# Optimization experiments

Hardware: AMD Instinct MI355X
Metric: run time of the kernel (lower is better)

The kernel has to match this reference:

```python
import jax, jax.numpy as jnp
import numpy as np

N = 4096; TD = 768; ID = 512; H = 256; NH = 4; HD = H // NH; NC = 3; E = 131072


def _gcn(x, w, b, src, dst, n):
    # GCNConv: add self loops, sym-normalize, aggregate at dst
    loop = jnp.arange(n)
    s = jnp.concatenate([src, loop])
    d = jnp.concatenate([dst, loop])
    deg = jax.ops.segment_sum(jnp.ones(s.shape[0], x.dtype), d, num_segments=n)
    dinv = jnp.where(deg > 0, jax.lax.rsqrt(deg), 0.0)
    norm = dinv[s] * dinv[d]                      # [E+N]
    h = x @ w                                     # [N,H] transform
    out = jax.ops.segment_sum(norm[:, None] * h[s], d, num_segments=n)
    return out + b


def setup_inputs() -> dict:
    key = jax.random.key(0)
    ks = jax.random.split(key, 20)
    p = lambda k, shp, sc: jax.random.normal(k, shp, jnp.float32) * sc
    inp = {
        "text_features": jax.random.normal(ks[0], (N, TD), jnp.float32),
        "image_features": jax.random.normal(ks[1], (N, ID), jnp.float32),
        "edge_index": jax.random.randint(ks[2], (2, E), 0, N, jnp.int32),
        "text_w": p(ks[3], (TD, H), 0.02), "text_b": jnp.zeros((H,), jnp.float32),
        "image_w": p(ks[4], (ID, H), 0.02), "image_b": jnp.zeros((H,), jnp.float32),
        "wq": p(ks[5], (H, H), 0.02), "bq": jnp.zeros((H,), jnp.float32),
        "wk": p(ks[6], (H, H), 0.02), "bk": jnp.zeros((H,), jnp.float32),
        "wv": p(ks[7], (H, H), 0.02), "bv": jnp.zeros((H,), jnp.float32),
        "wo": p(ks[8], (H, H), 0.02), "bo": jnp.zeros((H,), jnp.float32),
        "gcn1_w": p(ks[9], (H, H), 0.02), "gcn1_b": jnp.zeros((H,), jnp.float32),
        "gcn2_w": p(ks[10], (H, H), 0.02), "gcn2_b": jnp.zeros((H,), jnp.float32),
        "cls_w": p(ks[11], (H, NC), 0.02), "cls_b": jnp.zeros((NC,), jnp.float32),
    }
    return inp


def reference(text_features, image_features, edge_index,
              text_w, text_b, image_w, image_b,
              wq, bq, wk, bk, wv, bv, wo, bo,
              gcn1_w, gcn1_b, gcn2_w, gcn2_b, cls_w, cls_b):
    # fused linear+relu projections, then elementwise fuse of sum
    combined = (jax.nn.relu(text_features @ text_w + text_b)
                + jax.nn.relu(image_features @ image_w + image_b))  # [N,H]
    # MHA over all nodes (seq_len=N, batch=1)
    q = (combined @ wq + bq).reshape(N, NH, HD)
    k = (combined @ wk + bk).reshape(N, NH, HD)
    v = (combined @ wv + bv).reshape(N, NH, HD)
    scores = jnp.einsum('nhd,mhd->hnm', q, k) / jnp.sqrt(jnp.float32(HD))
    attn = jax.nn.softmax(scores, axis=-1)
    o = jnp.einsum('hnm,mhd->nhd', attn, v).reshape(N, H)
    attn_out = o @ wo + bo
    # two GCN layers
    src, dst = edge_index[0], edge_index[1]
    g1 = jax.nn.relu(_gcn(attn_out, gcn1_w, gcn1_b, src, dst, N))
    g2 = _gcn(g1, gcn2_w, gcn2_b, src, dst, N)
    return g2 @ cls_w + cls_b
```

## Files before the change

### kernel.cpp

```cpp
#include <hip/hip_runtime.h>
#include <hip/hip_bf16.h>

typedef unsigned short ushort;
typedef __attribute__((ext_vector_type(8))) short short8;
typedef __attribute__((ext_vector_type(4))) float f32x4;

constexpr int N_  = 4096;
constexpr int TD_ = 768;
constexpr int ID_ = 512;
constexpr int H_  = 256;
constexpr int HD_ = 64;
constexpr int E_  = 131072;
constexpr int SPLITS = 16;
constexpr float QSCALE = 0.125f * 1.44269504088896f;

#define MFMA16(a, b, c) __builtin_amdgcn_mfma_f32_16x16x32_bf16(a, b, c, 0, 0, 0)

__device__ inline ushort f2bf(float x) {
    union { float f; unsigned u; } v; v.f = x;
    unsigned r = v.u + 0x7fff + ((v.u >> 16) & 1);
    return (ushort)(r >> 16);
}
__device__ inline float lo2f(unsigned u) { union { unsigned x; float f; } v; v.x = u << 16; return v.f; }
__device__ inline float hi2f(unsigned u) { union { unsigned x; float f; } v; v.x = u & 0xffff0000u; return v.f; }

__device__ inline float exp2r(float x) {
    float r;
    asm("v_exp_f32 %0, %1" : "=v"(r) : "v"(x));
    return r;
}
__device__ inline unsigned pkbf(float lo, float hi) {
    union { float f; unsigned u; } a, b; a.f = lo; b.f = hi;
    return __builtin_amdgcn_perm(b.u + 0x8000u, a.u + 0x8000u, 0x07060302u);
}

__device__ inline void gl_lds16(const void* g, void* l) {
    __builtin_amdgcn_global_load_lds((const __attribute__((address_space(1))) unsigned int*)g,
                                     (__attribute__((address_space(3))) unsigned int*)l, 16, 0, 0);
}

__device__ inline void stage64(const ushort* g, long long strideEl, ushort* lds, int w, int l) {
    int r8 = l >> 3;
    int cc = (l & 7) ^ r8;
    #pragma unroll
    for (int p = 0; p < 2; p++) {
        int row = w * 16 + p * 8 + r8;
        gl_lds16(g + (long long)row * strideEl + cc * 8, lds + (w * 16 + p * 8) * 64);
    }
}
__device__ inline void stageB16(const ushort* g, long long strideEl, ushort* lds, int w, int l) {
    if (w < 2) {
        int r8 = l >> 3;
        int row = w * 8 + r8;
        int cc = (l & 7) ^ (row & 7);
        gl_lds16(g + (long long)row * strideEl + cc * 8, lds + w * 512);
    }
}
__device__ inline int swz(int row, int kOff) {
    return row * 64 + ((((kOff >> 3) ^ (row & 7))) << 3);
}


__global__ __launch_bounds__(256) void k_init(int* __restrict__ indeg, int* __restrict__ pos) {
    int i = blockIdx.x * 256 + threadIdx.x;
    indeg[i] = 0;
    pos[i] = 0;
}


__global__ __launch_bounds__(256) void k_prep(const float* __restrict__ text, const float* __restrict__ img,
                                              const float* __restrict__ tw, const float* __restrict__ iw,
                                              const float* __restrict__ wq, const float* __restrict__ wk,
                                              const float* __restrict__ wv, const float* __restrict__ wo,
                                              const float* __restrict__ g1w, const float* __restrict__ g2w,
                                              const int* __restrict__ edst, int* __restrict__ indeg,
                                              ushort* __restrict__ textbf, ushort* __restrict__ imgbf,
                                              ushort* __restrict__ wobf,
                                              ushort* __restrict__ twT, ushort* __restrict__ iwT,
                                              ushort* __restrict__ wqT, ushort* __restrict__ wkT,
                                              ushort* __restrict__ wvT, ushort* __restrict__ g1wT,
                                              ushort* __restrict__ g2wT) {
    __shared__ float Ts[64][65];
    const int b = blockIdx.x;
    const int t = threadIdx.x;
    if (b >= 2752) {
        int e = (b - 2752) * 256 + t;
        atomicAdd(&indeg[edst[e]], 1);
        return;
    }
    if (b < 2592) {
        size_t base = ((size_t)b * 256 + t) * 8;
        const size_t TXE = (size_t)N_ * TD_, IME = (size_t)N_ * ID_;
        const float* src; ushort* dst;
        if (base < TXE) { src = text + base; dst = textbf + base; }
        else if (base < TXE + IME) { src = img + (base - TXE); dst = imgbf + (base - TXE); }
        else { src = wo + (base - TXE - IME); dst = wobf + (base - TXE - IME); }
        float4 x = *(const float4*)src;
        float4 y = *(const float4*)(src + 4);
        ushort o[8] = { f2bf(x.x), f2bf(x.y), f2bf(x.z), f2bf(x.w),
                        f2bf(y.x), f2bf(y.y), f2bf(y.z), f2bf(y.w) };
        *(short8*)dst = *(const short8*)o;
        return;
    }
    int wb = b - 2592;
    const float* src; ushort* dst; int R, tile;
    if (wb < 48)       { src = tw;  dst = twT;  R = 768; tile = wb; }
    else if (wb < 80)  { src = iw;  dst = iwT;  R = 512; tile = wb - 48; }
    else if (wb < 96)  { src = wq;  dst = wqT;  R = 256; tile = wb - 80; }
    else if (wb < 112) { src = wk;  dst = wkT;  R = 256; tile = wb - 96; }
    else if (wb < 128) { src = wv;  dst = wvT;  R = 256; tile = wb - 112; }
    else if (wb < 144) { src = g1w; dst = g1wT; R = 256; tile = wb - 128; }
    else               { src = g2w; dst = g2wT; R = 256; tile = wb - 144; }
    const int r0 = (tile >> 2) * 64, c0 = (tile & 3) * 64;
    #pragma unroll
    for (int u = 0; u < 16; u++) {
        int lin = t + u * 256;
        int r = lin >> 6, c = lin & 63;
        Ts[r][c] = src[(size_t)(r0 + r) * 256 + c0 + c];
    }
    __syncthreads();
    #pragma unroll
    for (int u = 0; u < 16; u++) {
        int lin = t + u * 256;
        int c = lin >> 6, r = lin & 63;
        dst[(size_t)(c0 + c) * R + r0 + r] = f2bf(Ts[r][c]);
    }
}


__global__ __launch_bounds__(256, 4) void k_combined16(const ushort* __restrict__ text, const ushort* __restrict__ img,
                                                       const ushort* __restrict__ twT, const ushort* __restrict__ iwT,
                                                       const float* __restrict__ tb, const float* __restrict__ ib,
                                                       const int* __restrict__ indeg, int* __restrict__ offs,
                                                       float* __restrict__ dinv, ushort* __restrict__ out) {
    __shared__ ushort As[2][4096];
    __shared__ ushort Bs[2][1024];
    __shared__ ushort Cs[64 * 24];
    __shared__ int sums[256];
    const int b = blockIdx.x;
    const int t = threadIdx.x;
    if (b == 1024) {
        int v[16]; int ssum = 0; int base = t * 16;
        #pragma unroll
        for (int k2 = 0; k2 < 16; k2++) { v[k2] = indeg[base + k2]; ssum += v[k2]; }
        sums[t] = ssum;
        __syncthreads();
        for (int off = 1; off < 256; off <<= 1) {
            int x = (t >= off) ? sums[t - off] : 0;
            __syncthreads();
            sums[t] += x;
            __syncthreads();
        }
        int excl = sums[t] - ssum;
        #pragma unroll
        for (int k2 = 0; k2 < 16; k2++) {
            offs[base + k2] = excl;
            excl += v[k2];
            dinv[base + k2] = 1.f / sqrtf((float)(v[k2] + 1));
        }
        return;
    }
    const int bm = (b >> 4) * 64, bn = (b & 15) * 16;
    const int w = t >> 6, l = t & 63, q = l >> 4, i = l & 15;
    f32x4 acc1 = {0, 0, 0, 0}, acc2 = {0, 0, 0, 0};
    auto stC = [&](int c, int buf) {
        if (c < 12) {
            stage64(text + (size_t)bm * TD_ + c * 64, TD_, As[buf], w, l);
            stageB16(twT + (size_t)bn * TD_ + c * 64, TD_, Bs[buf], w, l);
        } else {
            stage64(img + (size_t)bm * ID_ + (c - 12) * 64, ID_, As[buf], w, l);
            stageB16(iwT + (size_t)bn * ID_ + (c - 12) * 64, ID_, Bs[buf], w, l);
        }
    };
    stC(0, 0);
    for (int c = 0; c < 20; c++) {
        __syncthreads();
        if (c + 1 < 20) stC(c + 1, (c + 1) & 1);
        const ushort* Ab = As[c & 1];
        const ushort* Bb = Bs[c & 1];
        #pragma unroll
        for (int kb = 0; kb < 2; kb++) {
            short8 af = *(const short8*)&Ab[swz(w * 16 + i, kb * 32 + q * 8)];
            short8 bfr = *(const short8*)&Bb[swz(i, kb * 32 + q * 8)];
            if (c < 12) acc1 = MFMA16(af, bfr, acc1);
            else        acc2 = MFMA16(af, bfr, acc2);
        }
    }
    __syncthreads();
    float b1 = tb[bn + i], b2 = ib[bn + i];
    #pragma unroll
    for (int r = 0; r < 4; r++) {
        float v = fmaxf(acc1[r] + b1, 0.f) + fmaxf(acc2[r] + b2, 0.f);
        Cs[(w * 16 + q * 4 + r) * 24 + i] = f2bf(v);
    }
    __syncthreads();
    if (t < 128) {
        int row = t >> 1, h8 = (t & 1) * 8;
        *(short8*)(out + (size_t)(bm + row) * H_ + bn + h8) = *(const short8*)&Cs[row * 24 + h8];
    }
}


__global__ __launch_bounds__(256) void k_qkv_scatfold(const ushort* __restrict__ A,
                                                      const ushort* __restrict__ WqT, const ushort* __restrict__ WkT,
                                                      const ushort* __restrict__ WvT,
                                                      const float* __restrict__ bq, const float* __restrict__ bk,
                                                      const float* __restrict__ bv,
                                                      ushort* __restrict__ Qg, ushort* __restrict__ Kg,
                                                      ushort* __restrict__ Vtg,
                                                      const int* __restrict__ esrc, const int* __restrict__ edst,
                                                      const int* __restrict__ offs, const float* __restrict__ dinv,
                                                      int* __restrict__ pos, int* __restrict__ ssrc,
                                                      float* __restrict__ swv,
                                                      const ushort* __restrict__ g1wT, const ushort* __restrict__ wobf,
                                                      const float* __restrict__ bo,
                                                      ushort* __restrict__ WpT, float* __restrict__ bp) {
    __shared__ ushort As[2][4096];
    __shared__ ushort Bs[2][4096];
    __shared__ ushort Cs[64 * 72];
    const int b = blockIdx.x;
    const int t = threadIdx.x;
    const int w = t >> 6, l = t & 63, q = l >> 4, i = l & 15;

    if (b >= 768) {
        if (b < 1280) {
            int e = (b - 768) * 256 + t;
            int s = esrc[e], d = edst[e];
            int p = atomicAdd(&pos[d], 1);
            int idx = offs[d] + p;
            ssrc[idx] = s;
            swv[idx] = dinv[s] * dinv[d];
            return;
        }
        if (b == 1296) {
            float acc = 0.f;
            const ushort* row = g1wT + (size_t)t * 256;
            for (int m8 = 0; m8 < 256; m8 += 8) {
                #pragma unroll
                for (int j = 0; j < 8; j++) acc += bo[m8 + j] * lo2f(((unsigned)row[m8 + j]) << 16);
            }
            bp[t] = acc;
            return;
        }
        const int f = b - 1280;
        const int bm = (f >> 2) * 64, bn = (f & 3) * 64;
        f32x4 acc[4];
        #pragma unroll
        for (int nt = 0; nt < 4; nt++) acc[nt] = (f32x4){0, 0, 0, 0};
        stage64(g1wT + (size_t)bm * H_, H_, As[0], w, l);
        stage64(wobf + (size_t)bn * H_, H_, Bs[0], w, l);
        for (int c = 0; c < 4; c++) {
            __syncthreads();
            if (c < 3) {
                stage64(g1wT + (size_t)bm * H_ + (c + 1) * 64, H_, As[(c + 1) & 1], w, l);
                stage64(wobf + (size_t)bn * H_ + (c + 1) * 64, H_, Bs[(c + 1) & 1], w, l);
            }
            const ushort* Ab = As[c & 1];
            const ushort* Bb = Bs[c & 1];
            #pragma unroll
            for (int kb = 0; kb < 2; kb++) {
                short8 af = *(const short8*)&Ab[swz(w * 16 + i, kb * 32 + q * 8)];
                #pragma unroll
                for (int nt = 0; nt < 4; nt++) {
                    short8 bfr = *(const short8*)&Bb[swz(nt * 16 + i, kb * 32 + q * 8)];
                    acc[nt] = MFMA16(af, bfr, acc[nt]);
                }
            }
        }
        __syncthreads();
        #pragma unroll
        for (int nt = 0; nt < 4; nt++)
            #pragma unroll
            for (int r = 0; r < 4; r++)
                Cs[(w * 16 + q * 4 + r) * 72 + nt * 16 + i] = f2bf(acc[nt][r]);
        __syncthreads();
        int rr = t >> 2, c16 = (t & 3) * 16;
        short8 v0 = *(const short8*)&Cs[rr * 72 + c16];
        short8 v1 = *(const short8*)&Cs[rr * 72 + c16 + 8];
        ushort* dstp = WpT + (size_t)(bm + rr) * H_ + bn + c16;
        *(short8*)dstp = v0;
        *(short8*)(dstp + 8) = v1;
        return;
    }

    const int z = b >> 8, rem = b & 255;
    const int bm = (rem >> 2) * 64, head = rem & 3;
    const ushort* WT = (z == 0) ? WqT : (z == 1) ? WkT : WvT;
    const float* bias = (z == 0) ? bq : (z == 1) ? bk : bv;
    f32x4 acc[4];
    #pragma unroll
    for (int nt = 0; nt < 4; nt++) acc[nt] = (f32x4){0, 0, 0, 0};

    stage64(A + (size_t)bm * H_, H_, As[0], w, l);
    stage64(WT + (size_t)(head * 64) * H_, H_, Bs[0], w, l);
    for (int c = 0; c < 4; c++) {
        __syncthreads();
        if (c < 3) {
            stage64(A + (size_t)bm * H_ + (c + 1) * 64, H_, As[(c + 1) & 1], w, l);
            stage64(WT + (size_t)(head * 64) * H_ + (c + 1) * 64, H_, Bs[(c + 1) & 1], w, l);
        }
        const ushort* Ab = As[c & 1];
        const ushort* Bb = Bs[c & 1];
        #pragma unroll
        for (int kb = 0; kb < 2; kb++) {
            short8 af = *(const short8*)&Ab[swz(w * 16 + i, kb * 32 + q * 8)];
            #pragma unroll
            for (int nt = 0; nt < 4; nt++) {
                short8 bfr = *(const short8*)&Bb[swz(nt * 16 + i, kb * 32 + q * 8)];
                acc[nt] = MFMA16(af, bfr, acc[nt]);
            }
        }
    }
    __syncthreads();
    #pragma unroll
    for (int nt = 0; nt < 4; nt++) {
        float bv_ = bias[head * 64 + nt * 16 + i];
        #pragma unroll
        for (int r = 0; r < 4; r++) {
            float v = acc[nt][r] + bv_;
            if (z == 0) v *= QSCALE;
            if (z < 2) Cs[(w * 16 + q * 4 + r) * 72 + nt * 16 + i] = f2bf(v);
            else       Cs[(nt * 16 + i) * 72 + w * 16 + q * 4 + r] = f2bf(v);
        }
    }
    __syncthreads();
    int rr = t >> 2, c16 = (t & 3) * 16;
    short8 v0 = *(const short8*)&Cs[rr * 72 + c16];
    short8 v1 = *(const short8*)&Cs[rr * 72 + c16 + 8];
    ushort* dst;
    if (z < 2) dst = ((z == 0) ? Qg : Kg) + (size_t)head * N_ * HD_ + (size_t)(bm + rr) * HD_ + c16;
    else       dst = Vtg + (size_t)head * HD_ * N_ + (size_t)rr * N_ + bm + c16;
    *(short8*)dst = v0;
    *(short8*)(dst + 8) = v1;
}


__global__ __launch_bounds__(256) void k_attn_mfma(const ushort* __restrict__ Qg, const ushort* __restrict__ Kg,
                                                   const ushort* __restrict__ Vtg, ushort* __restrict__ Op,
                                                   float* __restrict__ lp) {
    __shared__ ushort Ks[4096];
    __shared__ ushort Vs[4096];
    __shared__ ushort Ps[4][16 * 72];
    const int head = blockIdx.y, r0 = blockIdx.x * 128, z = blockIdx.z;
    const int t = threadIdx.x, w = t >> 6, l = t & 63, q = l >> 4, i = l & 15;
    const int rw = (i ^ (i >> 1)) & 7;
    ushort* Pw = &Ps[w][0];

    short8 qf[2][2];
    #pragma unroll
    for (int qt = 0; qt < 2; qt++)
        #pragma unroll
        for (int kb = 0; kb < 2; kb++)
            qf[qt][kb] = *(const short8*)(Qg + ((size_t)head * N_ + r0 + qt * 64 + w * 16 + i) * HD_ + kb * 32 + q * 8);

    f32x4 Oacc[2][4];
    float lacc[2] = {0.f, 0.f};
    #pragma unroll
    for (int qt = 0; qt < 2; qt++)
        #pragma unroll
        for (int dt = 0; dt < 4; dt++) Oacc[qt][dt] = (f32x4){0, 0, 0, 0};

    const int NT = 64 / SPLITS;
    const int cb0 = z * NT;
    for (int it = 0; it < NT; it++) {
        const int cb = cb0 + it;
        __syncthreads();
        stage64(Kg + ((size_t)head * N_ + (size_t)cb * 64) * HD_, HD_, Ks, w, l);
        stage64(Vtg + (size_t)head * HD_ * N_ + cb * 64, N_, Vs, w, l);
        __syncthreads();

        f32x4 St[2][4];
        #pragma unroll
        for (int qt = 0; qt < 2; qt++)
            #pragma unroll
            for (int kt = 0; kt < 4; kt++) St[qt][kt] = (f32x4){0, 0, 0, 0};
        #pragma unroll
        for (int kb = 0; kb < 2; kb++) {
            #pragma unroll
            for (int kt = 0; kt < 4; kt++) {
                short8 kf = *(const short8*)&Ks[swz(kt * 16 + i, kb * 32 + q * 8)];
                St[0][kt] = MFMA16(kf, qf[0][kb], St[0][kt]);
                St[1][kt] = MFMA16(kf, qf[1][kb], St[1][kt]);
            }
        }
        #pragma unroll
        for (int qt = 0; qt < 2; qt++) {
            #pragma unroll
            for (int kt = 0; kt < 4; kt++) {
                float p0 = exp2r(St[qt][kt][0]), p1 = exp2r(St[qt][kt][1]);
                float p2 = exp2r(St[qt][kt][2]), p3 = exp2r(St[qt][kt][3]);
                lacc[qt] += (p0 + p1) + (p2 + p3);
                int off = i * 72 + (((2 * kt + (q >> 1)) ^ rw) << 3) + ((q & 1) << 2);
                uint2 v; v.x = pkbf(p0, p1); v.y = pkbf(p2, p3);
                *(uint2*)&Pw[off] = v;
            }
            #pragma unroll
            for (int kb = 0; kb < 2; kb++) {
                short8 pf = *(const short8*)&Pw[i * 72 + (((4 * kb + q) ^ rw) << 3)];
                #pragma unroll
                for (int dt = 0; dt < 4; dt++) {
                    short8 vf = *(const short8*)&Vs[swz(dt * 16 + i, kb * 32 + q * 8)];
                    Oacc[qt][dt] = MFMA16(vf, pf, Oacc[qt][dt]);
                }
            }
        }
    }

    #pragma unroll
    for (int qt = 0; qt < 2; qt++) {
        lacc[qt] += __shfl_xor(lacc[qt], 16);
        lacc[qt] += __shfl_xor(lacc[qt], 32);
    }

    const size_t sh = ((size_t)z * 4 + head) * N_;
    #pragma unroll
    for (int qt = 0; qt < 2; qt++) {
        const int row = r0 + qt * 64 + w * 16 + i;
        #pragma unroll
        for (int dt = 0; dt < 4; dt++) {
            uint2 v;
            v.x = pkbf(Oacc[qt][dt][0], Oacc[qt][dt][1]);
            v.y = pkbf(Oacc[qt][dt][2], Oacc[qt][dt][3]);
            *(uint2*)&Op[(sh + row) * HD_ + dt * 16 + q * 4] = v;
        }
        if (l < 16) lp[sh + r0 + qt * 64 + w * 16 + l] = lacc[qt];
    }
}

__global__ __launch_bounds__(256) void k_attn_merge(const ushort* __restrict__ Op, const float* __restrict__ lp,
                                                    ushort* __restrict__ obuf) {
    const int t = threadIdx.x;
    const int idx = blockIdx.x * 16 + (t >> 4);
    const int h = idx >> 12, n = idx & 4095;
    const int d4 = (t & 15) * 4;
    float lsum = 0.f;
    float acc[4] = {0.f, 0.f, 0.f, 0.f};
    #pragma unroll
    for (int s = 0; s < SPLITS; s++) {
        size_t sh = ((size_t)s * 4 + h) * N_ + n;
        lsum += lp[sh];
        uint2 o4 = *(const uint2*)&Op[sh * HD_ + d4];
        acc[0] += lo2f(o4.x); acc[1] += hi2f(o4.x);
        acc[2] += lo2f(o4.y); acc[3] += hi2f(o4.y);
    }
    float inv = 1.f / lsum;
    uint2 res;
    res.x = pkbf(acc[0] * inv, acc[1] * inv);
    res.y = pkbf(acc[2] * inv, acc[3] * inv);
    *(uint2*)&obuf[(size_t)n * H_ + h * HD_ + d4] = res;
}


template <bool BIAS>
__global__ __launch_bounds__(256, 4) void k_gemm16(const ushort* __restrict__ A, const ushort* __restrict__ BT,
                                                   const float* __restrict__ bias, ushort* __restrict__ outb) {
    __shared__ ushort As[2][4096];
    __shared__ ushort Bs[2][1024];
    __shared__ ushort Cs[64 * 24];
    const int bm = blockIdx.x * 64, bn = blockIdx.y * 16;
    const int t = threadIdx.x, w = t >> 6, l = t & 63, q = l >> 4, i = l & 15;
    f32x4 acc = {0, 0, 0, 0};
    stage64(A + (size_t)bm * H_, H_, As[0], w, l);
    stageB16(BT + (size_t)bn * H_, H_, Bs[0], w, l);
    for (int c = 0; c < 4; c++) {
        __syncthreads();
        if (c < 3) {
            stage64(A + (size_t)bm * H_ + (c + 1) * 64, H_, As[(c + 1) & 1], w, l);
            stageB16(BT + (size_t)bn * H_ + (c + 1) * 64, H_, Bs[(c + 1) & 1], w, l);
        }
        const ushort* Ab = As[c & 1];
        const ushort* Bb = Bs[c & 1];
        #pragma unroll
        for (int kb = 0; kb < 2; kb++) {
            short8 af = *(const short8*)&Ab[swz(w * 16 + i, kb * 32 + q * 8)];
            short8 bfr = *(const short8*)&Bb[swz(i, kb * 32 + q * 8)];
            acc = MFMA16(af, bfr, acc);
        }
    }
    __syncthreads();
    float bb = BIAS ? bias[bn + i] : 0.f;
    #pragma unroll
    for (int r = 0; r < 4; r++)
        Cs[(w * 16 + q * 4 + r) * 24 + i] = f2bf(acc[r] + bb);
    __syncthreads();
    if (t < 128) {
        int row = t >> 1, h8 = (t & 1) * 8;
        *(short8*)(outb + (size_t)(bm + row) * H_ + bn + h8) = *(const short8*)&Cs[row * 24 + h8];
    }
}


__global__ __launch_bounds__(256) void k_agg1(const ushort* __restrict__ h, const int* __restrict__ ssrc,
                                              const float* __restrict__ sw, const int* __restrict__ offs,
                                              const int* __restrict__ indeg, const float* __restrict__ dinv,
                                              const float* __restrict__ bias, ushort* __restrict__ outb) {
    const int t = threadIdx.x;
    const int j = __builtin_amdgcn_readfirstlane(blockIdx.x * 4 + (t >> 6));
    const int d0 = (t & 63) * 4;
    float dj = dinv[j];
    uint2 hv = *(const uint2*)&h[(size_t)j * H_ + d0];
    float s2 = dj * dj;
    float a0 = s2 * lo2f(hv.x), a1 = s2 * hi2f(hv.x), a2 = s2 * lo2f(hv.y), a3 = s2 * hi2f(hv.y);
    int start = offs[j], cnt = indeg[j];
    for (int e = 0; e < cnt; e++) {
        int s = ssrc[start + e];
        float wg = sw[start + e];
        uint2 v = *(const uint2*)&h[(size_t)s * H_ + d0];
        a0 += wg * lo2f(v.x); a1 += wg * hi2f(v.x);
        a2 += wg * lo2f(v.y); a3 += wg * hi2f(v.y);
    }
    a0 = fmaxf(a0 + bias[d0], 0.f);
    a1 = fmaxf(a1 + bias[d0 + 1], 0.f);
    a2 = fmaxf(a2 + bias[d0 + 2], 0.f);
    a3 = fmaxf(a3 + bias[d0 + 3], 0.f);
    uint2 o;
    o.x = pkbf(a0, a1);
    o.y = pkbf(a2, a3);
    *(uint2*)&outb[(size_t)j * H_ + d0] = o;
}


__global__ __launch_bounds__(256) void k_aggcls(const ushort* __restrict__ h, const int* __restrict__ ssrc,
                                                const float* __restrict__ sw, const int* __restrict__ offs,
                                                const int* __restrict__ indeg, const float* __restrict__ dinv,
                                                const float* __restrict__ bias, const float* __restrict__ cw,
                                                const float* __restrict__ cb, float* __restrict__ out) {
    const int t = threadIdx.x;
    const int j = __builtin_amdgcn_readfirstlane(blockIdx.x * 4 + (t >> 6));
    const int lane = t & 63;
    const int d0 = lane * 4;
    float dj = dinv[j];
    uint2 hv = *(const uint2*)&h[(size_t)j * H_ + d0];
    float s2 = dj * dj;
    float a0 = s2 * lo2f(hv.x), a1 = s2 * hi2f(hv.x), a2 = s2 * lo2f(hv.y), a3 = s2 * hi2f(hv.y);
    int start = offs[j], cnt = indeg[j];
    for (int e = 0; e < cnt; e++) {
        int s = ssrc[start + e];
        float wg = sw[start + e];
        uint2 v = *(const uint2*)&h[(size_t)s * H_ + d0];
        a0 += wg * lo2f(v.x); a1 += wg * hi2f(v.x);
        a2 += wg * lo2f(v.y); a3 += wg * hi2f(v.y);
    }
    a0 += bias[d0]; a1 += bias[d0 + 1]; a2 += bias[d0 + 2]; a3 += bias[d0 + 3];
    float p0 = a0 * cw[d0 * 3 + 0] + a1 * cw[(d0 + 1) * 3 + 0]
             + a2 * cw[(d0 + 2) * 3 + 0] + a3 * cw[(d0 + 3) * 3 + 0];
    float p1 = a0 * cw[d0 * 3 + 1] + a1 * cw[(d0 + 1) * 3 + 1]
             + a2 * cw[(d0 + 2) * 3 + 1] + a3 * cw[(d0 + 3) * 3 + 1];
    float p2 = a0 * cw[d0 * 3 + 2] + a1 * cw[(d0 + 1) * 3 + 2]
             + a2 * cw[(d0 + 2) * 3 + 2] + a3 * cw[(d0 + 3) * 3 + 2];
    #pragma unroll
    for (int off = 32; off > 0; off >>= 1) {
        p0 += __shfl_xor(p0, off);
        p1 += __shfl_xor(p1, off);
        p2 += __shfl_xor(p2, off);
    }
    if (lane == 0) {
        out[j * 3 + 0] = p0 + cb[0];
        out[j * 3 + 1] = p1 + cb[1];
        out[j * 3 + 2] = p2 + cb[2];
    }
}


extern "C" void kernel_launch(void* const* d_in, const int* in_sizes, int n_in,
                              void* d_out, int out_size, void* d_ws, size_t ws_size,
                              hipStream_t stream) {
    const float* text = (const float*)d_in[0];
    const float* img  = (const float*)d_in[1];
    const int*   eidx = (const int*)d_in[2];
    const float* tw  = (const float*)d_in[3];
    const float* tb  = (const float*)d_in[4];
    const float* iw  = (const float*)d_in[5];
    const float* ib  = (const float*)d_in[6];
    const float* wq  = (const float*)d_in[7];
    const float* bq  = (const float*)d_in[8];
    const float* wk  = (const float*)d_in[9];
    const float* bk  = (const float*)d_in[10];
    const float* wv  = (const float*)d_in[11];
    const float* bv  = (const float*)d_in[12];
    const float* wo  = (const float*)d_in[13];
    const float* bo  = (const float*)d_in[14];
    const float* g1w = (const float*)d_in[15];
    const float* g1b = (const float*)d_in[16];
    const float* g2w = (const float*)d_in[17];
    const float* g2b = (const float*)d_in[18];
    const float* cw  = (const float*)d_in[19];
    const float* cbv = (const float*)d_in[20];

    char* W = (char*)d_ws;
    size_t cur = 0;
    auto alloc = [&](size_t sz) { char* p = W + cur; cur += (sz + 255) & ~(size_t)255; return p; };

    float* dinv  = (float*)alloc(N_ * 4);
    float* swv   = (float*)alloc(E_ * 4);
    int* indeg   = (int*)alloc(N_ * 4);
    int* offs    = (int*)alloc(N_ * 4);
    int* pos     = (int*)alloc(N_ * 4);
    int* ssrc    = (int*)alloc(E_ * 4);
    ushort* Qg   = (ushort*)alloc((size_t)N_ * H_ * 2);
    ushort* Kg   = (ushort*)alloc((size_t)N_ * H_ * 2);
    ushort* Vtg  = (ushort*)alloc((size_t)N_ * H_ * 2);
    ushort* obuf = (ushort*)alloc((size_t)N_ * H_ * 2);
    ushort* WpT  = (ushort*)alloc((size_t)H_ * H_ * 2);
    float* bp    = (float*)alloc(H_ * 4);
    ushort* g1wT = (ushort*)alloc((size_t)H_ * H_ * 2);
    ushort* g2wT = (ushort*)alloc((size_t)H_ * H_ * 2);
    ushort* wobf = (ushort*)alloc((size_t)H_ * H_ * 2);
    float* lp    = (float*)alloc((size_t)SPLITS * 4 * N_ * 4);
    char* S = W + cur;

    ushort* textbf = (ushort*)S;
    ushort* imgbf  = textbf + (size_t)N_ * TD_;
    ushort* twT    = imgbf + (size_t)N_ * ID_;
    ushort* iwT    = twT + (size_t)TD_ * H_;
    ushort* wqT    = iwT + (size_t)ID_ * H_;
    ushort* wkT    = wqT + (size_t)H_ * H_;
    ushort* wvT    = wkT + (size_t)H_ * H_;
    ushort* combbf = wvT + (size_t)H_ * H_;
    ushort* Op = (ushort*)S;
    ushort* hbuf  = (ushort*)S;
    ushort* g1b16 = (ushort*)(S + (size_t)2 * 1024 * 1024);
    ushort* hbuf2 = (ushort*)(S + (size_t)4 * 1024 * 1024);

    const int* esrc = eidx;
    const int* edst = eidx + E_;

    k_init<<<dim3(N_ / 256), dim3(256), 0, stream>>>(indeg, pos);
    k_prep<<<dim3(3264), dim3(256), 0, stream>>>(text, img, tw, iw, wq, wk, wv, wo, g1w, g2w,
                                                 edst, indeg,
                                                 textbf, imgbf, wobf, twT, iwT, wqT, wkT, wvT, g1wT, g2wT);
    k_combined16<<<dim3(1025), dim3(256), 0, stream>>>(textbf, imgbf, twT, iwT, tb, ib,
                                                       indeg, offs, dinv, combbf);
    k_qkv_scatfold<<<dim3(1297), dim3(256), 0, stream>>>(combbf, wqT, wkT, wvT, bq, bk, bv, Qg, Kg, Vtg,
                                                         esrc, edst, offs, dinv, pos, ssrc, swv,
                                                         g1wT, wobf, bo, WpT, bp);
    k_attn_mfma<<<dim3(32, 4, SPLITS), dim3(256), 0, stream>>>(Qg, Kg, Vtg, Op, lp);
    k_attn_merge<<<dim3(1024), dim3(256), 0, stream>>>(Op, lp, obuf);

    k_gemm16<true><<<dim3(64, 16), dim3(256), 0, stream>>>(obuf, WpT, bp, hbuf);
    k_agg1<<<dim3(N_ / 4), dim3(256), 0, stream>>>(hbuf, ssrc, swv, offs, indeg, dinv, g1b, g1b16);
    k_gemm16<false><<<dim3(64, 16), dim3(256), 0, stream>>>(g1b16, g2wT, nullptr, hbuf2);
    k_aggcls<<<dim3(N_ / 4), dim3(256), 0, stream>>>(hbuf2, ssrc, swv, offs, indeg, dinv, g2b, cw, cbv,
                                                     (float*)d_out);
}
```

Measured before the change: 228.6 us.

## Widen combined-projection GEMM tiles and double-buffer K staging in attention

The text/image projection GEMM now gives each block a 64x64 output tile instead of 64x16. That cuts the grid from 1024 to 256 blocks, so each A tile is staged once and reused across four MFMA column tiles rather than being reloaded by sixteen blocks. The attention kernel now double-buffers the K tile and stages V for the current block after the loop-top barrier. A new barrier sits before the P·V product, so the V load can overlap the QK^T MFMAs. The trade-offs are more accumulator registers and LDS in the GEMM, fewer blocks to fill the GPU, and an extra barrier per attention iteration.

```diff
diff --git a/kernel.cpp b/kernel.cpp
--- a/kernel.cpp
+++ b/kernel.cpp
@@ -128,18 +128,18 @@
 }
 
 
-__global__ __launch_bounds__(256, 4) void k_combined16(const ushort* __restrict__ text, const ushort* __restrict__ img,
-                                                       const ushort* __restrict__ twT, const ushort* __restrict__ iwT,
-                                                       const float* __restrict__ tb, const float* __restrict__ ib,
-                                                       const int* __restrict__ indeg, int* __restrict__ offs,
-                                                       float* __restrict__ dinv, ushort* __restrict__ out) {
+__global__ __launch_bounds__(256) void k_combined16(const ushort* __restrict__ text, const ushort* __restrict__ img,
+                                                    const ushort* __restrict__ twT, const ushort* __restrict__ iwT,
+                                                    const float* __restrict__ tb, const float* __restrict__ ib,
+                                                    const int* __restrict__ indeg, int* __restrict__ offs,
+                                                    float* __restrict__ dinv, ushort* __restrict__ out) {
     __shared__ ushort As[2][4096];
-    __shared__ ushort Bs[2][1024];
-    __shared__ ushort Cs[64 * 24];
+    __shared__ ushort Bs[2][4096];
+    __shared__ ushort Cs[64 * 72];
     __shared__ int sums[256];
     const int b = blockIdx.x;
     const int t = threadIdx.x;
-    if (b == 1024) {
+    if (b == 256) {
         int v[16]; int ssum = 0; int base = t * 16;
         #pragma unroll
         for (int k2 = 0; k2 < 16; k2++) { v[k2] = indeg[base + k2]; ssum += v[k2]; }
@@ -160,16 +160,18 @@
         }
         return;
     }
-    const int bm = (b >> 4) * 64, bn = (b & 15) * 16;
+    const int bm = (b >> 2) * 64, bn = (b & 3) * 64;
     const int w = t >> 6, l = t & 63, q = l >> 4, i = l & 15;
-    f32x4 acc1 = {0, 0, 0, 0}, acc2 = {0, 0, 0, 0};
+    f32x4 acc1[4], acc2[4];
+    #pragma unroll
+    for (int nt = 0; nt < 4; nt++) { acc1[nt] = (f32x4){0, 0, 0, 0}; acc2[nt] = (f32x4){0, 0, 0, 0}; }
     auto stC = [&](int c, int buf) {
         if (c < 12) {
             stage64(text + (size_t)bm * TD_ + c * 64, TD_, As[buf], w, l);
-            stageB16(twT + (size_t)bn * TD_ + c * 64, TD_, Bs[buf], w, l);
+            stage64(twT + (size_t)bn * TD_ + c * 64, TD_, Bs[buf], w, l);
         } else {
             stage64(img + (size_t)bm * ID_ + (c - 12) * 64, ID_, As[buf], w, l);
-            stageB16(iwT + (size_t)bn * ID_ + (c - 12) * 64, ID_, Bs[buf], w, l);
+            stage64(iwT + (size_t)bn * ID_ + (c - 12) * 64, ID_, Bs[buf], w, l);
         }
     };
     stC(0, 0);
@@ -181,23 +183,31 @@
         #pragma unroll
         for (int kb = 0; kb < 2; kb++) {
             short8 af = *(const short8*)&Ab[swz(w * 16 + i, kb * 32 + q * 8)];
-            short8 bfr = *(const short8*)&Bb[swz(i, kb * 32 + q * 8)];
-            if (c < 12) acc1 = MFMA16(af, bfr, acc1);
-            else        acc2 = MFMA16(af, bfr, acc2);
+            #pragma unroll
+            for (int nt = 0; nt < 4; nt++) {
+                short8 bfr = *(const short8*)&Bb[swz(nt * 16 + i, kb * 32 + q * 8)];
+                if (c < 12) acc1[nt] = MFMA16(af, bfr, acc1[nt]);
+                else        acc2[nt] = MFMA16(af, bfr, acc2[nt]);
+            }
         }
     }
     __syncthreads();
-    float b1 = tb[bn + i], b2 = ib[bn + i];
-    #pragma unroll
-    for (int r = 0; r < 4; r++) {
-        float v = fmaxf(acc1[r] + b1, 0.f) + fmaxf(acc2[r] + b2, 0.f);
-        Cs[(w * 16 + q * 4 + r) * 24 + i] = f2bf(v);
+    #pragma unroll
+    for (int nt = 0; nt < 4; nt++) {
+        float b1 = tb[bn + nt * 16 + i], b2 = ib[bn + nt * 16 + i];
+        #pragma unroll
+        for (int r = 0; r < 4; r++) {
+            float v = fmaxf(acc1[nt][r] + b1, 0.f) + fmaxf(acc2[nt][r] + b2, 0.f);
+            Cs[(w * 16 + q * 4 + r) * 72 + nt * 16 + i] = f2bf(v);
+        }
     }
     __syncthreads();
-    if (t < 128) {
-        int row = t >> 1, h8 = (t & 1) * 8;
-        *(short8*)(out + (size_t)(bm + row) * H_ + bn + h8) = *(const short8*)&Cs[row * 24 + h8];
-    }
+    int rr = t >> 2, c16 = (t & 3) * 16;
+    short8 v0 = *(const short8*)&Cs[rr * 72 + c16];
+    short8 v1 = *(const short8*)&Cs[rr * 72 + c16 + 8];
+    ushort* dstp = out + (size_t)(bm + rr) * H_ + bn + c16;
+    *(short8*)dstp = v0;
+    *(short8*)(dstp + 8) = v1;
 }
 
 
@@ -338,7 +348,7 @@
 __global__ __launch_bounds__(256) void k_attn_mfma(const ushort* __restrict__ Qg, const ushort* __restrict__ Kg,
                                                    const ushort* __restrict__ Vtg, ushort* __restrict__ Op,
                                                    float* __restrict__ lp) {
-    __shared__ ushort Ks[4096];
+    __shared__ ushort Ks[2][4096];
     __shared__ ushort Vs[4096];
     __shared__ ushort Ps[4][16 * 72];
     const int head = blockIdx.y, r0 = blockIdx.x * 128, z = blockIdx.z;
@@ -362,12 +372,17 @@
 
     const int NT = 64 / SPLITS;
     const int cb0 = z * NT;
+    const ushort* Kbase = Kg + (size_t)head * N_ * HD_;
+    const ushort* Vbase = Vtg + (size_t)head * HD_ * N_;
+
+    stage64(Kbase + (size_t)cb0 * 64 * HD_, HD_, Ks[0], w, l);
     for (int it = 0; it < NT; it++) {
         const int cb = cb0 + it;
         __syncthreads();
-        stage64(Kg + ((size_t)head * N_ + (size_t)cb * 64) * HD_, HD_, Ks, w, l);
-        stage64(Vtg + (size_t)head * HD_ * N_ + cb * 64, N_, Vs, w, l);
-        __syncthreads();
+        stage64(Vbase + cb * 64, N_, Vs, w, l);
+        if (it + 1 < NT)
+            stage64(Kbase + (size_t)(cb + 1) * 64 * HD_, HD_, Ks[(it + 1) & 1], w, l);
+        const ushort* Kb = Ks[it & 1];
 
         f32x4 St[2][4];
         #pragma unroll
@@ -378,30 +393,46 @@
         for (int kb = 0; kb < 2; kb++) {
             #pragma unroll
             for (int kt = 0; kt < 4; kt++) {
-                short8 kf = *(const short8*)&Ks[swz(kt * 16 + i, kb * 32 + q * 8)];
+                short8 kf = *(const short8*)&Kb[swz(kt * 16 + i, kb * 32 + q * 8)];
                 St[0][kt] = MFMA16(kf, qf[0][kb], St[0][kt]);
                 St[1][kt] = MFMA16(kf, qf[1][kb], St[1][kt]);
             }
         }
         #pragma unroll
-        for (int qt = 0; qt < 2; qt++) {
-            #pragma unroll
-            for (int kt = 0; kt < 4; kt++) {
-                float p0 = exp2r(St[qt][kt][0]), p1 = exp2r(St[qt][kt][1]);
-                float p2 = exp2r(St[qt][kt][2]), p3 = exp2r(St[qt][kt][3]);
-                lacc[qt] += (p0 + p1) + (p2 + p3);
-                int off = i * 72 + (((2 * kt + (q >> 1)) ^ rw) << 3) + ((q & 1) << 2);
-                uint2 v; v.x = pkbf(p0, p1); v.y = pkbf(p2, p3);
-                *(uint2*)&Pw[off] = v;
-            }
-            #pragma unroll
-            for (int kb = 0; kb < 2; kb++) {
-                short8 pf = *(const short8*)&Pw[i * 72 + (((4 * kb + q) ^ rw) << 3)];
-                #pragma unroll
-                for (int dt = 0; dt < 4; dt++) {
-                    short8 vf = *(const short8*)&Vs[swz(dt * 16 + i, kb * 32 + q * 8)];
-                    Oacc[qt][dt] = MFMA16(vf, pf, Oacc[qt][dt]);
-                }
+        for (int kt = 0; kt < 4; kt++) {
+            float p0 = exp2r(St[0][kt][0]), p1 = exp2r(St[0][kt][1]);
+            float p2 = exp2r(St[0][kt][2]), p3 = exp2r(St[0][kt][3]);
+            lacc[0] += (p0 + p1) + (p2 + p3);
+            int off = i * 72 + (((2 * kt + (q >> 1)) ^ rw) << 3) + ((q & 1) << 2);
+            uint2 v; v.x = pkbf(p0, p1); v.y = pkbf(p2, p3);
+            *(uint2*)&Pw[off] = v;
+        }
+        __syncthreads();
+        #pragma unroll
+        for (int kb = 0; kb < 2; kb++) {
+            short8 pf = *(const short8*)&Pw[i * 72 + (((4 * kb + q) ^ rw) << 3)];
+            #pragma unroll
+            for (int dt = 0; dt < 4; dt++) {
+                short8 vf = *(const short8*)&Vs[swz(dt * 16 + i, kb * 32 + q * 8)];
+                Oacc[0][dt] = MFMA16(vf, pf, Oacc[0][dt]);
+            }
+        }
+        #pragma unroll
+        for (int kt = 0; kt < 4; kt++) {
+            float p0 = exp2r(St[1][kt][0]), p1 = exp2r(St[1][kt][1]);
+            float p2 = exp2r(St[1][kt][2]), p3 = exp2r(St[1][kt][3]);
+            lacc[1] += (p0 + p1) + (p2 + p3);
+            int off = i * 72 + (((2 * kt + (q >> 1)) ^ rw) << 3) + ((q & 1) << 2);
+            uint2 v; v.x = pkbf(p0, p1); v.y = pkbf(p2, p3);
+            *(uint2*)&Pw[off] = v;
+        }
+        #pragma unroll
+        for (int kb = 0; kb < 2; kb++) {
+            short8 pf = *(const short8*)&Pw[i * 72 + (((4 * kb + q) ^ rw) << 3)];
+            #pragma unroll
+            for (int dt = 0; dt < 4; dt++) {
+                short8 vf = *(const short8*)&Vs[swz(dt * 16 + i, kb * 32 + q * 8)];
+                Oacc[1][dt] = MFMA16(vf, pf, Oacc[1][dt]);
             }
         }
     }
@@ -629,8 +660,8 @@
     k_prep<<<dim3(3264), dim3(256), 0, stream>>>(text, img, tw, iw, wq, wk, wv, wo, g1w, g2w,
                                                  edst, indeg,
                                                  textbf, imgbf, wobf, twT, iwT, wqT, wkT, wvT, g1wT, g2wT);
-    k_combined16<<<dim3(1025), dim3(256), 0, stream>>>(textbf, imgbf, twT, iwT, tb, ib,
-                                                       indeg, offs, dinv, combbf);
+    k_combined16<<<dim3(257), dim3(256), 0, stream>>>(textbf, imgbf, twT, iwT, tb, ib,
+                                                      indeg, offs, dinv, combbf);
     k_qkv_scatfold<<<dim3(1297), dim3(256), 0, stream>>>(combbf, wqT, wkT, wvT, bq, bk, bv, Qg, Kg, Vtg,
                                                          esrc, edst, offs, dinv, pos, ssrc, swv,
                                                          g1wT, wobf, bo, WpT, bp);
```

New measurement: 236.5 us. 1.03x slower.
